# Kernel optimization log

Measured on AMD Instinct MI355X. Metric: run time of the kernel, lower is better.

## Reference

```python
import jax, jax.numpy as jnp
import numpy as np

P_DROP = 0.6  # F.dropout default training=True in the original forward

def setup_inputs() -> dict:
    key = jax.random.key(0)
    k1, k2, k3, k4 = jax.random.split(key, 4)
    B, T, V, F, K, O = 32, 12, 1000, 64, 3, 64
    x = jax.random.normal(k1, (B, T, V, F), dtype=jnp.float32)
    Att = jax.random.uniform(k2, (V, V), dtype=jnp.float32)
    cheb = jax.random.normal(k3, (K, V, V), dtype=jnp.float32)   # Chebyshev polynomials T_k(L)
    Theta = jax.random.normal(k4, (K, F, O), dtype=jnp.float32)  # per-order feature transforms
    return {"x": x, "Att": Att, "cheb": cheb, "Theta": Theta}

def reference(x, Att, cheb, Theta):
    # x: [B,T,V,F]; Att: [V,V]; cheb: [K,V,V]; Theta: [K,F,O]
    B, T, V, F = x.shape
    K = cheb.shape[0]
    keep = 1.0 - P_DROP
    # Original draws a fresh dropout mask per (time_step, k); replicate with a fixed key.
    mask = jax.random.bernoulli(jax.random.key(42), keep, (T, K, V, V))
    TkA = cheb * Att                                   # [K,V,V] attention-weighted polynomial
    M = jnp.where(mask, TkA[None] / keep, 0.0)         # [T,K,V,V] inverted dropout
    # rhs = T_k_with_at @ graph_signal, batched over (b,t,k)
    rhs = jnp.einsum('tkuv,btvf->btkuf', M, x)         # [B,T,K,V,F]
    # sum_k rhs_k @ Theta_k  -> [B,T,V,O]; matches permute(0,3,1,2) of stacked outputs
    out = jnp.einsum('btkuf,kfo->btuo', rhs, Theta)
    return jax.nn.relu(out)
```

## Files before the change

kernel.cpp:

```cpp
#include <hip/hip_runtime.h>
#include <hip/hip_bf16.h>
#include <stdint.h>


typedef __attribute__((ext_vector_type(8))) short short8;
typedef __attribute__((ext_vector_type(4))) float f32x4;

__device__ __forceinline__ ushort f2bf(float f) {
  __hip_bfloat16 h = __float2bfloat16(f);
  return *reinterpret_cast<ushort*>(&h);
}

__device__ __forceinline__ void threefry2x32(uint32_t c0, uint32_t c1,
                                             uint32_t& o0, uint32_t& o1) {
  const uint32_t ks0 = 0u;
  const uint32_t ks1 = 42u;
  const uint32_t ks2 = ks0 ^ ks1 ^ 0x1BD11BDAu;
  uint32_t x0 = c0 + ks0;
  uint32_t x1 = c1 + ks1;
#define TFR(r) { x0 += x1; x1 = (x1 << (r)) | (x1 >> (32 - (r))); x1 ^= x0; }
  TFR(13) TFR(15) TFR(26) TFR(6)
  x0 += ks1; x1 += ks2 + 1u;
  TFR(17) TFR(29) TFR(16) TFR(24)
  x0 += ks2; x1 += ks0 + 2u;
  TFR(13) TFR(15) TFR(26) TFR(6)
  x0 += ks0; x1 += ks1 + 3u;
  TFR(17) TFR(29) TFR(16) TFR(24)
  x0 += ks1; x1 += ks2 + 4u;
  TFR(13) TFR(15) TFR(26) TFR(6)
  x0 += ks2; x1 += ks0 + 5u;
#undef TFR
  o0 = x0; o1 = x1;
}

__global__ void build_m(const float* __restrict__ Att,
                        const float* __restrict__ cheb,
                        ushort* __restrict__ Mws) {
  const uint32_t idx = blockIdx.x * 256u + threadIdx.x;
  const uint32_t vp = idx & 1023u;
  const uint32_t up = (idx >> 10) & 1023u;
  const uint32_t tk = idx >> 20;
  float val = 0.f;
  if ((vp < 1000u) & (up < 1000u)) {
    const uint32_t flat = (tk * 1000u + up) * 1000u + vp;
    uint32_t o0, o1;
    threefry2x32(0u, flat, o0, o1);
    const uint32_t bits = o0 ^ o1;
    const float u = __uint_as_float((bits >> 9) | 0x3f800000u) - 1.0f;
    if (u < 0.4f) {
      val = cheb[(tk % 3u) * 1000000u + up * 1000u + vp] *
            Att[up * 1000u + vp] * 2.5f;
    }
  }
  Mws[idx] = f2bf(val);
}

__global__ void transpose_x(const float* __restrict__ x,
                            ushort* __restrict__ xt) {
  __shared__ float lt[64][65];
  const int vc = blockIdx.x, t = blockIdx.y, b = blockIdx.z;
  const int tid = threadIdx.x;
  const int v0 = vc * 64;
#pragma unroll
  for (int i = 0; i < 4; ++i) {
    const int c = i * 256 + tid;
    const int vi = c >> 4, f4 = c & 15;
    float4 q = make_float4(0.f, 0.f, 0.f, 0.f);
    if (v0 + vi < 1000)
      q = *(const float4*)(x + ((((size_t)b * 12 + t) * 1000 + v0 + vi) << 6) + f4 * 4);
    lt[f4 * 4 + 0][vi] = q.x;
    lt[f4 * 4 + 1][vi] = q.y;
    lt[f4 * 4 + 2][vi] = q.z;
    lt[f4 * 4 + 3][vi] = q.w;
  }
  __syncthreads();
  const int f = tid >> 2, g = tid & 3;
  alignas(16) ushort tmp[16];
#pragma unroll
  for (int j = 0; j < 16; ++j) tmp[j] = f2bf(lt[f][g * 16 + j]);
  const size_t base = ((size_t)(t * 2048 + b * 64 + f)) << 10;
  *(uint4*)(xt + base + v0 + g * 16)     = *(const uint4*)&tmp[0];
  *(uint4*)(xt + base + v0 + g * 16 + 8) = *(const uint4*)&tmp[8];
}

#define LDT 72

#define MFMA(a, b, c) __builtin_amdgcn_mfma_f32_16x16x32_bf16((a), (b), (c), 0, 0, 0)

#define STAGE_LOAD(P0, P1, P2, P3, P4, P5, P6, P7, CO)                        \
  do {                                                                        \
    P0 = *(const uint4*)(Mws + ga0 + (CO));                                   \
    P1 = *(const uint4*)(Mws + ga1 + (CO));                                   \
    P2 = *(const uint4*)(Mws + ga0 + 1048576 + (CO));                         \
    P3 = *(const uint4*)(Mws + ga1 + 1048576 + (CO));                         \
    P4 = *(const uint4*)(Mws + ga0 + 2097152 + (CO));                         \
    P5 = *(const uint4*)(Mws + ga1 + 2097152 + (CO));                         \
    P6 = *(const uint4*)(xt + gx0 + (CO));                                    \
    P7 = *(const uint4*)(xt + gx1 + (CO));                                    \
  } while (0)

#define STAGE_WRITE(P0, P1, P2, P3, P4, P5, P6, P7, BP)                       \
  do {                                                                        \
    *(uint4*)&(BP)[da0]         = P0;                                         \
    *(uint4*)&(BP)[da1]         = P1;                                         \
    *(uint4*)&(BP)[8192 + da0]  = P2;                                         \
    *(uint4*)&(BP)[8192 + da1]  = P3;                                         \
    *(uint4*)&(BP)[16384 + da0] = P4;                                         \
    *(uint4*)&(BP)[16384 + da1] = P5;                                         \
    *(uint4*)&(BP)[24576 + da0] = P6;                                         \
    *(uint4*)&(BP)[24576 + da1] = P7;                                         \
  } while (0)

#define BURST(BP)                                                             \
  do {                                                                        \
    const ushort* sAc = (BP);                                                 \
    const ushort* sBc = (BP) + 24576;                                         \
    _Pragma("unroll")                                                         \
    for (int ks = 0; ks < 2; ++ks) {                                          \
      short8 bv[4];                                                           \
      _Pragma("unroll")                                                       \
      for (int ni = 0; ni < 4; ++ni) {                                        \
        const int row = wn * 64 + ni * 16 + l15;                              \
        bv[ni] = *(const short8*)&sBc[row * 64 + (((ks * 4 + quad) ^ rsw) * 8)]; \
      }                                                                       \
      _Pragma("unroll")                                                       \
      for (int k = 0; k < 3; ++k) {                                           \
        short8 av[2];                                                         \
        _Pragma("unroll")                                                     \
        for (int mi = 0; mi < 2; ++mi) {                                      \
          const int row = wu * 32 + mi * 16 + l15;                            \
          av[mi] = *(const short8*)&sAc[k * 8192 + row * 64 +                 \
                                        (((ks * 4 + quad) ^ rsw) * 8)];       \
        }                                                                     \
        _Pragma("unroll")                                                     \
        for (int mi = 0; mi < 2; ++mi)                                        \
          _Pragma("unroll")                                                   \
          for (int ni = 0; ni < 4; ++ni)                                      \
            pacc[k][mi][ni] = MFMA(av[mi], bv[ni], pacc[k][mi][ni]);          \
      }                                                                       \
    }                                                                         \
  } while (0)

__global__ __launch_bounds__(512, 2)
void cheb_main(const ushort* __restrict__ Mws, const ushort* __restrict__ xt,
               const float* __restrict__ Theta, float* __restrict__ out) {
  __shared__ __align__(16) ushort smem[65536];
  const int tid = threadIdx.x;
  const int lane = tid & 63;
  const int w = tid >> 6;
  const int wu = w >> 1, wn = w & 1;
  const int quad = lane >> 4, l15 = lane & 15;
  const int nt = blockIdx.x, ut = blockIdx.y, t = blockIdx.z;
  const int u0 = ut * 128, n0 = nt * 128;

  ushort* buf0 = smem;
  ushort* buf1 = smem + 32768;
  ushort* sP  = smem + w * (32 * LDT);
  ushort* sTh = smem + 24576;

  const int srow = lane >> 3;
  const int gchunk = (lane & 7) ^ srow;
  const int rsw = l15 & 7;

  const size_t mbase = (size_t)(t * 3) << 20;
  const size_t xrow0 = (size_t)(t * 2048 + n0);

  const int rr0 = 8 * (w * 2 + 0) + srow;
  const int rr1 = 8 * (w * 2 + 1) + srow;
  const size_t ga0 = mbase + ((size_t)(u0 + rr0) << 10) + gchunk * 8;
  const size_t ga1 = mbase + ((size_t)(u0 + rr1) << 10) + gchunk * 8;
  const size_t gx0 = ((xrow0 + rr0) << 10) + gchunk * 8;
  const size_t gx1 = ((xrow0 + rr1) << 10) + gchunk * 8;
  const int da0 = (w * 2 + 0) * 512 + lane * 8;
  const int da1 = (w * 2 + 1) * 512 + lane * 8;

  f32x4 pacc[3][2][4];
#pragma unroll
  for (int k = 0; k < 3; ++k)
#pragma unroll
    for (int i = 0; i < 2; ++i)
#pragma unroll
      for (int j = 0; j < 4; ++j) pacc[k][i][j] = f32x4{0.f, 0.f, 0.f, 0.f};

  uint4 p0, p1, p2, p3, p4, p5, p6, p7;
  uint4 q0, q1, q2, q3, q4, q5, q6, q7;

  STAGE_LOAD(q0, q1, q2, q3, q4, q5, q6, q7, 0);
  STAGE_LOAD(p0, p1, p2, p3, p4, p5, p6, p7, 64);
  STAGE_WRITE(q0, q1, q2, q3, q4, q5, q6, q7, buf0);
  __syncthreads();

#pragma unroll 1
  for (int it = 0; it < 8; ++it) {
    const int vc = it * 2;
    __builtin_amdgcn_s_setprio(1);
    BURST(buf0);
    __builtin_amdgcn_s_setprio(0);
    if (vc < 15) STAGE_WRITE(p0, p1, p2, p3, p4, p5, p6, p7, buf1);
    if (vc < 14) STAGE_LOAD(q0, q1, q2, q3, q4, q5, q6, q7, (size_t)(vc + 2) * 64);
    __syncthreads();
    __builtin_amdgcn_s_setprio(1);
    BURST(buf1);
    __builtin_amdgcn_s_setprio(0);
    if (vc + 1 < 15) STAGE_WRITE(q0, q1, q2, q3, q4, q5, q6, q7, buf0);
    if (vc + 1 < 14) STAGE_LOAD(p0, p1, p2, p3, p4, p5, p6, p7, (size_t)(vc + 3) * 64);
    __syncthreads();
  }

  f32x4 oacc[2][4];
#pragma unroll
  for (int i = 0; i < 2; ++i)
#pragma unroll
    for (int j = 0; j < 4; ++j) oacc[i][j] = f32x4{0.f, 0.f, 0.f, 0.f};

#pragma unroll
  for (int k = 0; k < 3; ++k) {
    __syncthreads();
#pragma unroll
    for (int mi = 0; mi < 2; ++mi)
#pragma unroll
      for (int ni = 0; ni < 4; ++ni)
#pragma unroll
        for (int r = 0; r < 4; ++r)
          sP[(mi * 16 + quad * 4 + r) * LDT + ni * 16 + l15] = f2bf(pacc[k][mi][ni][r]);
    for (int e = tid; e < 4096; e += 512) {
      const int f = e >> 6, o = e & 63;
      sTh[o * LDT + f] = f2bf(Theta[k * 4096 + e]);
    }
    __syncthreads();
#pragma unroll
    for (int ks = 0; ks < 2; ++ks) {
      short8 a2[2], b2[4];
#pragma unroll
      for (int mi = 0; mi < 2; ++mi)
        a2[mi] = *(const short8*)&sP[(mi * 16 + l15) * LDT + ks * 32 + quad * 8];
#pragma unroll
      for (int ni = 0; ni < 4; ++ni)
        b2[ni] = *(const short8*)&sTh[(ni * 16 + l15) * LDT + ks * 32 + quad * 8];
#pragma unroll
      for (int mi = 0; mi < 2; ++mi)
#pragma unroll
        for (int ni = 0; ni < 4; ++ni)
          oacc[mi][ni] = MFMA(a2[mi], b2[ni], oacc[mi][ni]);
    }
  }

#pragma unroll
  for (int mi = 0; mi < 2; ++mi) {
    const int u_base = u0 + wu * 32 + mi * 16 + quad * 4;
#pragma unroll
    for (int ni = 0; ni < 4; ++ni) {
      const int n = n0 + wn * 64 + ni * 16 + l15;
      const int b = n >> 6, oo = n & 63;
      float* op = out + (((size_t)b * 12 + t) * 1000) * 64 + oo;
#pragma unroll
      for (int r = 0; r < 4; ++r) {
        const int u = u_base + r;
        if (u < 1000) op[(size_t)u * 64] = fmaxf(oacc[mi][ni][r], 0.f);
      }
    }
  }
}

extern "C" void kernel_launch(void* const* d_in, const int* in_sizes, int n_in,
                              void* d_out, int out_size, void* d_ws, size_t ws_size,
                              hipStream_t stream) {
  const float* x     = (const float*)d_in[0];
  const float* Att   = (const float*)d_in[1];
  const float* cheb  = (const float*)d_in[2];
  const float* Theta = (const float*)d_in[3];
  float* out = (float*)d_out;

  ushort* Mws = (ushort*)d_ws;
  ushort* xtw = Mws + 37748736ull;

  build_m<<<147456, 256, 0, stream>>>(Att, cheb, Mws);
  transpose_x<<<dim3(16, 12, 32), 256, 0, stream>>>(x, xtw);
  cheb_main<<<dim3(16, 8, 12), 512, 0, stream>>>(Mws, xtw, Theta, out);
}
```

Measured before the change: 286.9 us.

## Shrink main GEMM tile to 64 rows, single-buffer LDS, swizzle block order

Halves the u-tile from 128 to 64 rows and the block from 512 to 256 threads. Replaces the double-buffered LDS ring with a single 40KB buffer plus register prefetch of the next chunk, and remaps a flat grid of 3072 blocks with an XCD-aware swizzle. The aim is more resident blocks per CU and better L2 locality across XCDs. In exchange, the x tile is reloaded twice as often and every step needs an extra barrier.

```diff
diff --git a/kernel.cpp b/kernel.cpp
--- a/kernel.cpp
+++ b/kernel.cpp
@@ -87,51 +87,52 @@
 
 #define MFMA(a, b, c) __builtin_amdgcn_mfma_f32_16x16x32_bf16((a), (b), (c), 0, 0, 0)
 
-#define STAGE_LOAD(P0, P1, P2, P3, P4, P5, P6, P7, CO)                        \
+#define LOADCH(R0, R1, R2, R3, R4, R5, R6, R7, R8, R9, VC)                    \
   do {                                                                        \
-    P0 = *(const uint4*)(Mws + ga0 + (CO));                                   \
-    P1 = *(const uint4*)(Mws + ga1 + (CO));                                   \
-    P2 = *(const uint4*)(Mws + ga0 + 1048576 + (CO));                         \
-    P3 = *(const uint4*)(Mws + ga1 + 1048576 + (CO));                         \
-    P4 = *(const uint4*)(Mws + ga0 + 2097152 + (CO));                         \
-    P5 = *(const uint4*)(Mws + ga1 + 2097152 + (CO));                         \
-    P6 = *(const uint4*)(xt + gx0 + (CO));                                    \
-    P7 = *(const uint4*)(xt + gx1 + (CO));                                    \
+    const size_t co_ = (size_t)(VC) * 64;                                     \
+    R0 = *(const uint4*)(Mws + aS0 + co_);                                    \
+    R1 = *(const uint4*)(Mws + aS1 + co_);                                    \
+    R2 = *(const uint4*)(Mws + aS2 + co_);                                    \
+    R3 = *(const uint4*)(Mws + aS3 + co_);                                    \
+    R4 = *(const uint4*)(Mws + aS4 + co_);                                    \
+    R5 = *(const uint4*)(Mws + aS5 + co_);                                    \
+    R6 = *(const uint4*)(xt + bS0 + co_);                                     \
+    R7 = *(const uint4*)(xt + bS1 + co_);                                     \
+    R8 = *(const uint4*)(xt + bS2 + co_);                                     \
+    R9 = *(const uint4*)(xt + bS3 + co_);                                     \
   } while (0)
 
-#define STAGE_WRITE(P0, P1, P2, P3, P4, P5, P6, P7, BP)                       \
+#define WRITECH(R0, R1, R2, R3, R4, R5, R6, R7, R8, R9)                       \
   do {                                                                        \
-    *(uint4*)&(BP)[da0]         = P0;                                         \
-    *(uint4*)&(BP)[da1]         = P1;                                         \
-    *(uint4*)&(BP)[8192 + da0]  = P2;                                         \
-    *(uint4*)&(BP)[8192 + da1]  = P3;                                         \
-    *(uint4*)&(BP)[16384 + da0] = P4;                                         \
-    *(uint4*)&(BP)[16384 + da1] = P5;                                         \
-    *(uint4*)&(BP)[24576 + da0] = P6;                                         \
-    *(uint4*)&(BP)[24576 + da1] = P7;                                         \
+    *(uint4*)&smem[(tid) * 8]                = R0;                            \
+    *(uint4*)&smem[(256 + tid) * 8]          = R1;                            \
+    *(uint4*)&smem[(512 + tid) * 8]          = R2;                            \
+    *(uint4*)&smem[(768 + tid) * 8]          = R3;                            \
+    *(uint4*)&smem[(1024 + tid) * 8]         = R4;                            \
+    *(uint4*)&smem[(1280 + tid) * 8]         = R5;                            \
+    *(uint4*)&smem[12288 + (tid) * 8]        = R6;                            \
+    *(uint4*)&smem[12288 + (256 + tid) * 8]  = R7;                            \
+    *(uint4*)&smem[12288 + (512 + tid) * 8]  = R8;                            \
+    *(uint4*)&smem[12288 + (768 + tid) * 8]  = R9;                            \
   } while (0)
 
-#define BURST(BP)                                                             \
+#define BURST()                                                               \
   do {                                                                        \
-    const ushort* sAc = (BP);                                                 \
-    const ushort* sBc = (BP) + 24576;                                         \
     _Pragma("unroll")                                                         \
     for (int ks = 0; ks < 2; ++ks) {                                          \
+      const int cs_ = (((ks * 4 + quad) ^ rsw)) << 3;                         \
       short8 bv[4];                                                           \
       _Pragma("unroll")                                                       \
-      for (int ni = 0; ni < 4; ++ni) {                                        \
-        const int row = wn * 64 + ni * 16 + l15;                              \
-        bv[ni] = *(const short8*)&sBc[row * 64 + (((ks * 4 + quad) ^ rsw) * 8)]; \
-      }                                                                       \
+      for (int ni = 0; ni < 4; ++ni)                                          \
+        bv[ni] = *(const short8*)&smem[12288 +                                \
+                     (wn * 64 + ni * 16 + l15) * 64 + cs_];                   \
       _Pragma("unroll")                                                       \
       for (int k = 0; k < 3; ++k) {                                           \
         short8 av[2];                                                         \
         _Pragma("unroll")                                                     \
-        for (int mi = 0; mi < 2; ++mi) {                                      \
-          const int row = wu * 32 + mi * 16 + l15;                            \
-          av[mi] = *(const short8*)&sAc[k * 8192 + row * 64 +                 \
-                                        (((ks * 4 + quad) ^ rsw) * 8)];       \
-        }                                                                     \
+        for (int mi = 0; mi < 2; ++mi)                                        \
+          av[mi] = *(const short8*)&smem[k * 4096 +                           \
+                       (wu * 32 + mi * 16 + l15) * 64 + cs_];                 \
         _Pragma("unroll")                                                     \
         for (int mi = 0; mi < 2; ++mi)                                        \
           _Pragma("unroll")                                                   \
@@ -141,38 +142,48 @@
     }                                                                         \
   } while (0)
 
-__global__ __launch_bounds__(512, 2)
+__global__ __launch_bounds__(256, 2)
 void cheb_main(const ushort* __restrict__ Mws, const ushort* __restrict__ xt,
                const float* __restrict__ Theta, float* __restrict__ out) {
-  __shared__ __align__(16) ushort smem[65536];
+  __shared__ __align__(16) ushort smem[20480];
   const int tid = threadIdx.x;
   const int lane = tid & 63;
   const int w = tid >> 6;
   const int wu = w >> 1, wn = w & 1;
   const int quad = lane >> 4, l15 = lane & 15;
-  const int nt = blockIdx.x, ut = blockIdx.y, t = blockIdx.z;
-  const int u0 = ut * 128, n0 = nt * 128;
-
-  ushort* buf0 = smem;
-  ushort* buf1 = smem + 32768;
-  ushort* sP  = smem + w * (32 * LDT);
-  ushort* sTh = smem + 24576;
-
-  const int srow = lane >> 3;
-  const int gchunk = (lane & 7) ^ srow;
   const int rsw = l15 & 7;
+
+  const int bid = blockIdx.x;
+  const int swz = (bid & 7) * 384 + (bid >> 3);
+  const int ut = swz & 15;
+  const int g = swz >> 4;
+  const int nt = g & 15;
+  const int t = g >> 4;
+  const int u0 = ut * 64, n0 = nt * 128;
 
   const size_t mbase = (size_t)(t * 3) << 20;
   const size_t xrow0 = (size_t)(t * 2048 + n0);
 
-  const int rr0 = 8 * (w * 2 + 0) + srow;
-  const int rr1 = 8 * (w * 2 + 1) + srow;
-  const size_t ga0 = mbase + ((size_t)(u0 + rr0) << 10) + gchunk * 8;
-  const size_t ga1 = mbase + ((size_t)(u0 + rr1) << 10) + gchunk * 8;
-  const size_t gx0 = ((xrow0 + rr0) << 10) + gchunk * 8;
-  const size_t gx1 = ((xrow0 + rr1) << 10) + gchunk * 8;
-  const int da0 = (w * 2 + 0) * 512 + lane * 8;
-  const int da1 = (w * 2 + 1) * 512 + lane * 8;
+  const int rA0 = tid >> 3,           cA0 = (tid & 7) ^ (rA0 & 7);
+  const int rA1 = (256 + tid) >> 3 & 63, cA1 = (tid & 7) ^ (rA1 & 7);
+  const int rA2 = tid >> 3,           cA2 = cA0;
+  const int rA3 = rA1,                cA3 = cA1;
+  const int rA4 = tid >> 3,           cA4 = cA0;
+  const int rA5 = rA1,                cA5 = cA1;
+  const size_t aS0 = mbase + ((size_t)(u0 + rA0) << 10) + cA0 * 8;
+  const size_t aS1 = mbase + ((size_t)(u0 + rA1) << 10) + cA1 * 8;
+  const size_t aS2 = mbase + (1ull << 20) + ((size_t)(u0 + rA2) << 10) + cA2 * 8;
+  const size_t aS3 = mbase + (1ull << 20) + ((size_t)(u0 + rA3) << 10) + cA3 * 8;
+  const size_t aS4 = mbase + (2ull << 20) + ((size_t)(u0 + rA4) << 10) + cA4 * 8;
+  const size_t aS5 = mbase + (2ull << 20) + ((size_t)(u0 + rA5) << 10) + cA5 * 8;
+  const int rB0 = tid >> 3,           cB0 = (tid & 7) ^ (rB0 & 7);
+  const int rB1 = (256 + tid) >> 3,   cB1 = (tid & 7) ^ (rB1 & 7);
+  const int rB2 = (512 + tid) >> 3,   cB2 = (tid & 7) ^ (rB2 & 7);
+  const int rB3 = (768 + tid) >> 3,   cB3 = (tid & 7) ^ (rB3 & 7);
+  const size_t bS0 = ((xrow0 + rB0) << 10) + cB0 * 8;
+  const size_t bS1 = ((xrow0 + rB1) << 10) + cB1 * 8;
+  const size_t bS2 = ((xrow0 + rB2) << 10) + cB2 * 8;
+  const size_t bS3 = ((xrow0 + rB3) << 10) + cB3 * 8;
 
   f32x4 pacc[3][2][4];
 #pragma unroll
@@ -182,31 +193,27 @@
 #pragma unroll
       for (int j = 0; j < 4; ++j) pacc[k][i][j] = f32x4{0.f, 0.f, 0.f, 0.f};
 
-  uint4 p0, p1, p2, p3, p4, p5, p6, p7;
-  uint4 q0, q1, q2, q3, q4, q5, q6, q7;
-
-  STAGE_LOAD(q0, q1, q2, q3, q4, q5, q6, q7, 0);
-  STAGE_LOAD(p0, p1, p2, p3, p4, p5, p6, p7, 64);
-  STAGE_WRITE(q0, q1, q2, q3, q4, q5, q6, q7, buf0);
+  uint4 p0, p1, p2, p3, p4, p5, p6, p7, p8, p9;
+
+  LOADCH(p0, p1, p2, p3, p4, p5, p6, p7, p8, p9, 0);
+  WRITECH(p0, p1, p2, p3, p4, p5, p6, p7, p8, p9);
   __syncthreads();
 
 #pragma unroll 1
-  for (int it = 0; it < 8; ++it) {
-    const int vc = it * 2;
+  for (int vc = 0; vc < 16; ++vc) {
+    if (vc < 15) LOADCH(p0, p1, p2, p3, p4, p5, p6, p7, p8, p9, vc + 1);
     __builtin_amdgcn_s_setprio(1);
-    BURST(buf0);
+    BURST();
     __builtin_amdgcn_s_setprio(0);
-    if (vc < 15) STAGE_WRITE(p0, p1, p2, p3, p4, p5, p6, p7, buf1);
-    if (vc < 14) STAGE_LOAD(q0, q1, q2, q3, q4, q5, q6, q7, (size_t)(vc + 2) * 64);
     __syncthreads();
-    __builtin_amdgcn_s_setprio(1);
-    BURST(buf1);
-    __builtin_amdgcn_s_setprio(0);
-    if (vc + 1 < 15) STAGE_WRITE(q0, q1, q2, q3, q4, q5, q6, q7, buf0);
-    if (vc + 1 < 14) STAGE_LOAD(p0, p1, p2, p3, p4, p5, p6, p7, (size_t)(vc + 3) * 64);
-    __syncthreads();
-  }
-
+    if (vc < 15) {
+      WRITECH(p0, p1, p2, p3, p4, p5, p6, p7, p8, p9);
+      __syncthreads();
+    }
+  }
+
+  ushort* sP  = smem + w * 2304;
+  ushort* sTh = smem + 9216;
   f32x4 oacc[2][4];
 #pragma unroll
   for (int i = 0; i < 2; ++i)
@@ -223,7 +230,7 @@
 #pragma unroll
         for (int r = 0; r < 4; ++r)
           sP[(mi * 16 + quad * 4 + r) * LDT + ni * 16 + l15] = f2bf(pacc[k][mi][ni][r]);
-    for (int e = tid; e < 4096; e += 512) {
+    for (int e = tid; e < 4096; e += 256) {
       const int f = e >> 6, o = e & 63;
       sTh[o * LDT + f] = f2bf(Theta[k * 4096 + e]);
     }
@@ -276,5 +283,5 @@
 
   build_m<<<147456, 256, 0, stream>>>(Att, cheb, Mws);
   transpose_x<<<dim3(16, 12, 32), 256, 0, stream>>>(x, xtw);
-  cheb_main<<<dim3(16, 8, 12), 512, 0, stream>>>(Mws, xtw, Theta, out);
-}
+  cheb_main<<<3072, 256, 0, stream>>>(Mws, xtw, Theta, out);
+}
```

Result: no change. 283.4 us (-1.2%).
